# Performance work log

Measured on AMD Instinct MI355X. Metric: run time of the kernel, lower is better.

Reference implementation:

```python
import jax, jax.numpy as jnp
import numpy as np

F_NODES = 16384   # number of function nodes
DEG = 8           # in-degree == out-degree per function node
E = F_NODES * DEG # edge-latent dimension (num edges)
B = 64            # batch
H = 16            # hidden_channels of each per-node MLP
LAYERS = 10       # GSNN layers (weights shared across layers)


def setup_inputs() -> dict:
    key = jax.random.key(0)
    k0, k1, k2, k3 = jax.random.split(key, 4)
    x0 = jax.random.normal(k0, (B, E), dtype=jnp.float32)
    # each edge has exactly one destination function node -> in_ixs is a permutation of edges
    in_ixs = jax.random.permutation(k1, E).reshape(F_NODES, DEG)
    # per-node 2-layer MLP weights: in_degree -> H -> out_degree
    W1 = jax.random.normal(k2, (F_NODES, H, DEG), dtype=jnp.float32) * (1.0 / np.sqrt(DEG))
    b1 = jnp.zeros((F_NODES, H), dtype=jnp.float32)
    W2 = jax.random.normal(k3, (F_NODES, DEG, H), dtype=jnp.float32) * (1.0 / np.sqrt(H))
    b2 = jnp.zeros((F_NODES, DEG), dtype=jnp.float32)
    return {"x0": x0, "W1": W1, "b1": b1, "W2": W2, "b2": b2, "in_ixs": in_ixs}


def reference(x0, W1, b1, W2, b2, in_ixs):
    # x0: [B, E] edge-latent input. Each layer: every function node gathers its
    # in-edges, applies its own small MLP, scatters to its out-edges; results are
    # summed into x_new and a residual x0 is added (GSNN.forward).
    x = x0
    for _ in range(LAYERS):
        g = x[:, in_ixs]                                   # [B, F, DEG] gather in-edge values
        h = jax.nn.elu(jnp.einsum('bfd,fhd->bfh', g, W1) + b1)  # [B, F, H]
        o = jnp.einsum('bfh,foh->bfo', h, W2) + b2         # [B, F, DEG]
        # out-edges of node f are the contiguous slots f*DEG:(f+1)*DEG (disjoint scatter)
        x = o.reshape(x0.shape) + x0                       # sum of node scatters + residual
    return x
```

## Files before the change

### kernel.cpp

```cpp
#include <hip/hip_runtime.h>
#include <math.h>

#define F_NODES 16384
#define DEG 8
#define E_TOT (F_NODES * DEG)
#define B 64
#define H 16
#define LAYERS 10
#define NPW 2

typedef unsigned short bf16_t;

__device__ __forceinline__ bf16_t f32_to_bf16(float f)
{
    unsigned u = __float_as_uint(f);
    u = (u + 0x7FFFu + ((u >> 16) & 1u)) >> 16;
    return (bf16_t)u;
}
__device__ __forceinline__ float bf16_to_f32(bf16_t h)
{
    return __uint_as_float((unsigned)h << 16);
}

__global__ __launch_bounds__(256) void transpose_in_kernel(
    const float* __restrict__ x0, float* __restrict__ xT,
    bf16_t* __restrict__ xT16)
{
    __shared__ float tile[64 * 65];
    const int e0 = blockIdx.x * 64;
    const int c  = threadIdx.x & 63;
    const int r  = threadIdx.x >> 6;

    #pragma unroll
    for (int i = 0; i < 16; ++i) {
        const int b = r + i * 4;
        tile[c * 65 + b] = x0[(size_t)b * E_TOT + e0 + c];
    }
    __syncthreads();
    const int b = threadIdx.x & 63;
    #pragma unroll
    for (int i = 0; i < 16; ++i) {
        const int el = r + i * 4;
        const float v = tile[el * 65 + b];
        const size_t idx = (size_t)(e0 + el) * B + b;
        xT[idx]   = v;
        xT16[idx] = f32_to_bf16(v);
    }
}

__global__ __launch_bounds__(256) void build_inv_kernel(
    const int* __restrict__ in_ixs, int* __restrict__ inv)
{
    const int k = blockIdx.x * 256 + threadIdx.x;
    inv[in_ixs[k]] = k;
}

__device__ __forceinline__ float fast_elu(float x)
{
    float e = __builtin_amdgcn_exp2f(x * 1.44269504088896340736f) - 1.0f;
    return x > 0.0f ? x : e;
}

template <int MODE>
__global__ __launch_bounds__(256) void layer_kernel(
    const bf16_t* __restrict__ zin,
    const float*  __restrict__ x0T,
    const bf16_t* __restrict__ x0T16,
    const float*  __restrict__ W1,
    const float*  __restrict__ b1,
    const float*  __restrict__ W2,
    const float*  __restrict__ b2,
    const int*    __restrict__ in_ixs,
    const int*    __restrict__ inv,
    bf16_t* __restrict__ zout,
    float*  __restrict__ out)
{
    const int lane    = threadIdx.x & 63;
    const int wv      = threadIdx.x >> 6;
    const int wave_id = (int)blockIdx.x * 4 + wv;

    #pragma unroll
    for (int n = 0; n < NPW; ++n) {
        const int f = __builtin_amdgcn_readfirstlane(wave_id * NPW + n);

        float g[DEG], r[DEG];
        if (MODE == 0) {
            const int* ixp = in_ixs + f * DEG;
            const float* rp = x0T + (size_t)f * DEG * B + lane;
            #pragma unroll
            for (int d = 0; d < DEG; ++d) {
                g[d] = x0T[(size_t)ixp[d] * B + lane];
                r[d] = rp[d * B];
            }
        } else if (MODE == 1) {
            const bf16_t* zp  = zin   + (size_t)f * DEG * B + lane;
            const bf16_t* rp  = x0T16 + (size_t)f * DEG * B + lane;
            #pragma unroll
            for (int d = 0; d < DEG; ++d) {
                g[d] = bf16_to_f32(zp[d * B]);
                r[d] = bf16_to_f32(rp[d * B]);
            }
        } else {
            const bf16_t* zp = zin + (size_t)f * DEG * B + lane;
            const float*  rp = x0T + (size_t)f * DEG * B + lane;
            #pragma unroll
            for (int d = 0; d < DEG; ++d) {
                g[d] = bf16_to_f32(zp[d * B]);
                r[d] = rp[d * B];
            }
        }

        const float* w1  = W1 + f * (H * DEG);
        const float* bb1 = b1 + f * H;
        float h[H];
        #pragma unroll
        for (int j = 0; j < H; ++j) {
            float acc = bb1[j];
            #pragma unroll
            for (int d = 0; d < DEG; ++d)
                acc = fmaf(w1[j * DEG + d], g[d], acc);
            h[j] = fast_elu(acc);
        }

        const float* w2  = W2 + f * (DEG * H);
        const float* bb2 = b2 + f * DEG;
        float o[DEG];
        #pragma unroll
        for (int d = 0; d < DEG; ++d) {
            float acc = bb2[d];
            #pragma unroll
            for (int j = 0; j < H; ++j)
                acc = fmaf(w2[d * H + j], h[j], acc);
            o[d] = acc + r[d];
        }

        if (MODE == 2) {
            float4 v0 = make_float4(o[0], o[1], o[2], o[3]);
            float4 v1 = make_float4(o[4], o[5], o[6], o[7]);
            float4* dst = (float4*)(out + (size_t)lane * E_TOT + f * DEG);
            dst[0] = v0;
            dst[1] = v1;
        } else {
            const int* invp = inv + f * DEG;
            #pragma unroll
            for (int d = 0; d < DEG; ++d)
                zout[(size_t)invp[d] * B + lane] = f32_to_bf16(o[d]);
        }
    }
}

extern "C" void kernel_launch(void* const* d_in, const int* in_sizes, int n_in,
                              void* d_out, int out_size, void* d_ws, size_t ws_size,
                              hipStream_t stream)
{
    const float* x0     = (const float*)d_in[0];
    const float* W1     = (const float*)d_in[1];
    const float* b1     = (const float*)d_in[2];
    const float* W2     = (const float*)d_in[3];
    const float* b2     = (const float*)d_in[4];
    const int*   in_ixs = (const int*)d_in[5];
    float* out = (float*)d_out;

    const size_t NEL = (size_t)E_TOT * B;
    float*  x0T   = (float*)d_ws;
    bf16_t* x0T16 = (bf16_t*)(x0T + NEL);
    bf16_t* zA    = x0T16 + NEL;
    bf16_t* zB    = zA + NEL;
    int*    inv   = (int*)(zB + NEL);

    transpose_in_kernel<<<E_TOT / 64, 256, 0, stream>>>(x0, x0T, x0T16);
    build_inv_kernel<<<E_TOT / 256, 256, 0, stream>>>(in_ixs, inv);

    const int grid = F_NODES / (4 * NPW);

    layer_kernel<0><<<grid, 256, 0, stream>>>(
        nullptr, x0T, x0T16, W1, b1, W2, b2, in_ixs, inv, zA, nullptr);

    const bf16_t* cur = zA;
    bf16_t* nxt = zB;
    for (int l = 1; l < LAYERS - 1; ++l) {
        layer_kernel<1><<<grid, 256, 0, stream>>>(
            cur, x0T, x0T16, W1, b1, W2, b2, in_ixs, inv, nxt, nullptr);
        cur = nxt;
        nxt = (nxt == zA) ? zB : zA;
    }

    layer_kernel<2><<<grid, 256, 0, stream>>>(
        cur, x0T, x0T16, W1, b1, W2, b2, in_ixs, inv, nullptr, out);
}
```

Baseline: 325.8 us.

## Pack weights to bf16 and drop the fp32 transposed input copy

Adds a pre-pass that converts W1 and W2 to packed bf16 pairs, so each layer reads half as many weight bytes, unpacked with shifts and masks. The fp32 transposed copy of x0 is removed, and the first and last layers now read the bf16 residual and gather source. This cuts memory traffic in the transpose and in every layer. In exchange it adds a weight-conversion kernel on each call and lowers the precision of the weights and of the residual in the first and final layers.

```diff
diff --git a/kernel.cpp b/kernel.cpp
--- a/kernel.cpp
+++ b/kernel.cpp
@@ -21,10 +21,11 @@
 {
     return __uint_as_float((unsigned)h << 16);
 }
+__device__ __forceinline__ float bfu_lo(unsigned u) { return __uint_as_float(u << 16); }
+__device__ __forceinline__ float bfu_hi(unsigned u) { return __uint_as_float(u & 0xFFFF0000u); }
 
 __global__ __launch_bounds__(256) void transpose_in_kernel(
-    const float* __restrict__ x0, float* __restrict__ xT,
-    bf16_t* __restrict__ xT16)
+    const float* __restrict__ x0, bf16_t* __restrict__ xT16)
 {
     __shared__ float tile[64 * 65];
     const int e0 = blockIdx.x * 64;
@@ -41,10 +42,7 @@
     #pragma unroll
     for (int i = 0; i < 16; ++i) {
         const int el = r + i * 4;
-        const float v = tile[el * 65 + b];
-        const size_t idx = (size_t)(e0 + el) * B + b;
-        xT[idx]   = v;
-        xT16[idx] = f32_to_bf16(v);
+        xT16[(size_t)(e0 + el) * B + b] = f32_to_bf16(tile[el * 65 + b]);
     }
 }
 
@@ -55,6 +53,17 @@
     inv[in_ixs[k]] = k;
 }
 
+__global__ __launch_bounds__(256) void pack_weights_kernel(
+    const float* __restrict__ W1, const float* __restrict__ W2,
+    unsigned* __restrict__ W1b, unsigned* __restrict__ W2b)
+{
+    const int i = blockIdx.x * 256 + threadIdx.x;
+    float2 a = ((const float2*)W1)[i];
+    W1b[i] = (unsigned)f32_to_bf16(a.x) | ((unsigned)f32_to_bf16(a.y) << 16);
+    float2 c = ((const float2*)W2)[i];
+    W2b[i] = (unsigned)f32_to_bf16(c.x) | ((unsigned)f32_to_bf16(c.y) << 16);
+}
+
 __device__ __forceinline__ float fast_elu(float x)
 {
     float e = __builtin_amdgcn_exp2f(x * 1.44269504088896340736f) - 1.0f;
@@ -63,15 +72,14 @@
 
 template <int MODE>
 __global__ __launch_bounds__(256) void layer_kernel(
-    const bf16_t* __restrict__ zin,
-    const float*  __restrict__ x0T,
-    const bf16_t* __restrict__ x0T16,
-    const float*  __restrict__ W1,
-    const float*  __restrict__ b1,
-    const float*  __restrict__ W2,
-    const float*  __restrict__ b2,
-    const int*    __restrict__ in_ixs,
-    const int*    __restrict__ inv,
+    const bf16_t*  __restrict__ zin,
+    const bf16_t*  __restrict__ x0T16,
+    const unsigned* __restrict__ W1b,
+    const float*   __restrict__ b1,
+    const unsigned* __restrict__ W2b,
+    const float*   __restrict__ b2,
+    const int*     __restrict__ in_ixs,
+    const int*     __restrict__ inv,
     bf16_t* __restrict__ zout,
     float*  __restrict__ out)
 {
@@ -84,53 +92,52 @@
         const int f = __builtin_amdgcn_readfirstlane(wave_id * NPW + n);
 
         float g[DEG], r[DEG];
-        if (MODE == 0) {
-            const int* ixp = in_ixs + f * DEG;
-            const float* rp = x0T + (size_t)f * DEG * B + lane;
-            #pragma unroll
-            for (int d = 0; d < DEG; ++d) {
-                g[d] = x0T[(size_t)ixp[d] * B + lane];
-                r[d] = rp[d * B];
+        {
+            const bf16_t* rp = x0T16 + (size_t)f * DEG * B + lane;
+            if (MODE == 0) {
+                const int* ixp = in_ixs + f * DEG;
+                #pragma unroll
+                for (int d = 0; d < DEG; ++d) {
+                    g[d] = bf16_to_f32(x0T16[(size_t)ixp[d] * B + lane]);
+                    r[d] = bf16_to_f32(rp[d * B]);
+                }
+            } else {
+                const bf16_t* zp = zin + (size_t)f * DEG * B + lane;
+                #pragma unroll
+                for (int d = 0; d < DEG; ++d) {
+                    g[d] = bf16_to_f32(zp[d * B]);
+                    r[d] = bf16_to_f32(rp[d * B]);
+                }
             }
-        } else if (MODE == 1) {
-            const bf16_t* zp  = zin   + (size_t)f * DEG * B + lane;
-            const bf16_t* rp  = x0T16 + (size_t)f * DEG * B + lane;
-            #pragma unroll
-            for (int d = 0; d < DEG; ++d) {
-                g[d] = bf16_to_f32(zp[d * B]);
-                r[d] = bf16_to_f32(rp[d * B]);
-            }
-        } else {
-            const bf16_t* zp = zin + (size_t)f * DEG * B + lane;
-            const float*  rp = x0T + (size_t)f * DEG * B + lane;
-            #pragma unroll
-            for (int d = 0; d < DEG; ++d) {
-                g[d] = bf16_to_f32(zp[d * B]);
-                r[d] = rp[d * B];
-            }
-        }
-
-        const float* w1  = W1 + f * (H * DEG);
-        const float* bb1 = b1 + f * H;
+        }
+
+        const unsigned* w1 = W1b + f * (H * DEG / 2);
+        const float*   bb1 = b1 + f * H;
         float h[H];
         #pragma unroll
         for (int j = 0; j < H; ++j) {
             float acc = bb1[j];
             #pragma unroll
-            for (int d = 0; d < DEG; ++d)
-                acc = fmaf(w1[j * DEG + d], g[d], acc);
+            for (int dp = 0; dp < DEG / 2; ++dp) {
+                const unsigned u = w1[j * (DEG / 2) + dp];
+                acc = fmaf(bfu_lo(u), g[2 * dp],     acc);
+                acc = fmaf(bfu_hi(u), g[2 * dp + 1], acc);
+            }
             h[j] = fast_elu(acc);
         }
 
-        const float* w2  = W2 + f * (DEG * H);
-        const float* bb2 = b2 + f * DEG;
+        const unsigned* w2 = W2b + f * (DEG * H / 2);
+        const float*   bb2 = b2 + f * DEG;
         float o[DEG];
         #pragma unroll
         for (int d = 0; d < DEG; ++d) {
             float acc = bb2[d];
             #pragma unroll
-            for (int j = 0; j < H; ++j)
-                acc = fmaf(w2[d * H + j], h[j], acc);
+            for (int jp = 0; jp < H / 2; ++jp) {
+                const unsigned u = w2[d * (H / 2) + jp];
+                acc = fmaf(bfu_lo(u), h[2 * jp],     acc);
+                acc = fmaf(bfu_hi(u), h[2 * jp + 1], acc);
+            }
             o[d] = acc + r[d];
         }
 
@@ -162,29 +169,32 @@
     float* out = (float*)d_out;
 
     const size_t NEL = (size_t)E_TOT * B;
-    float*  x0T   = (float*)d_ws;
-    bf16_t* x0T16 = (bf16_t*)(x0T + NEL);
-    bf16_t* zA    = x0T16 + NEL;
-    bf16_t* zB    = zA + NEL;
-    int*    inv   = (int*)(zB + NEL);
-
-    transpose_in_kernel<<<E_TOT / 64, 256, 0, stream>>>(x0, x0T, x0T16);
+    bf16_t*   x0T16 = (bf16_t*)d_ws;
+    bf16_t*   zA    = x0T16 + NEL;
+    bf16_t*   zB    = zA + NEL;
+    int*      inv   = (int*)(zB + NEL);
+    unsigned* W1b   = (unsigned*)(inv + E_TOT);
+    unsigned* W2b   = W1b + F_NODES * H * DEG / 2;
+
+    transpose_in_kernel<<<E_TOT / 64, 256, 0, stream>>>(x0, x0T16);
     build_inv_kernel<<<E_TOT / 256, 256, 0, stream>>>(in_ixs, inv);
+    pack_weights_kernel<<<F_NODES * H * DEG / 2 / 256, 256, 0, stream>>>(
+        W1, W2, W1b, W2b);
 
     const int grid = F_NODES / (4 * NPW);
 
     layer_kernel<0><<<grid, 256, 0, stream>>>(
-        nullptr, x0T, x0T16, W1, b1, W2, b2, in_ixs, inv, zA, nullptr);
+        nullptr, x0T16, W1b, b1, W2b, b2, in_ixs, inv, zA, nullptr);
 
     const bf16_t* cur = zA;
     bf16_t* nxt = zB;
     for (int l = 1; l < LAYERS - 1; ++l) {
         layer_kernel<1><<<grid, 256, 0, stream>>>(
-            cur, x0T, x0T16, W1, b1, W2, b2, in_ixs, inv, nxt, nullptr);
+            cur, x0T16, W1b, b1, W2b, b2, in_ixs, inv, nxt, nullptr);
         cur = nxt;
         nxt = (nxt == zA) ? zB : zA;
     }
 
     layer_kernel<2><<<grid, 256, 0, stream>>>(
-        cur, x0T, x0T16, W1, b1, W2, b2, in_ixs, inv, nullptr, out);
-}
+        cur, x0T16, W1b, b1, W2b, b2, in_ixs, inv, nullptr, out);
+}
```

Result: faster. 295.0 us (-9.5%).
